# Kernel tuning notes

Hardware: AMD Instinct MI355X
Metric: run time of the kernel (lower is better)

Reference implementation:

```python
import jax, jax.numpy as jnp
import numpy as np

NUM_EXPERTS = 8
TOP_K = 2
HIDDEN = 1024
INTER = 4096
LB_WEIGHT = 0.01


def setup_inputs() -> dict:
    key = jax.random.key(0)
    ks = jax.random.split(key, 6)
    s = 0.02
    return {
        "hidden_states": jax.random.normal(ks[0], (2, 2048, HIDDEN), dtype=jnp.float32),
        "Wg": jax.random.normal(ks[1], (HIDDEN, NUM_EXPERTS), dtype=jnp.float32) * s,
        "w1": jax.random.normal(ks[2], (NUM_EXPERTS, HIDDEN, INTER), dtype=jnp.float32) * s,
        "b1": jnp.zeros((NUM_EXPERTS, INTER), dtype=jnp.float32),
        "w2": jax.random.normal(ks[3], (NUM_EXPERTS, INTER, HIDDEN), dtype=jnp.float32) * s,
        "b2": jnp.zeros((NUM_EXPERTS, HIDDEN), dtype=jnp.float32),
    }


def reference(hidden_states, Wg, w1, b1, w2, b2):
    B, S, H = hidden_states.shape
    x = hidden_states.reshape(-1, H)            # [T, H]
    T = x.shape[0]

    # 1. Gating: softmax over experts, top-k selection, renormalized gates
    probs = jax.nn.softmax(x @ Wg, axis=-1)     # [T, E]
    top_v, top_i = jax.lax.top_k(probs, TOP_K)  # [T, K]
    gate = top_v / jnp.sum(top_v, axis=-1, keepdims=True)

    # Load-balancing aux loss: E * sum(frac_assigned * mean_prob) * weight
    frac = jnp.mean(jax.nn.one_hot(top_i, NUM_EXPERTS, dtype=probs.dtype), axis=(0, 1))  # [E]
    mean_p = jnp.mean(probs, axis=0)            # [E]
    aux_loss = NUM_EXPERTS * jnp.sum(frac * mean_p) * LB_WEIGHT

    # Combine weights: per-token weight for each expert (sum of matching top-k gates)
    combine = jnp.zeros((T, NUM_EXPERTS), dtype=x.dtype)
    combine = combine.at[jnp.arange(T)[:, None], top_i].add(gate)  # [T, E]

    # 2-4. Expert FFN + weighted combine (math-equivalent dense-per-expert form)
    out = jnp.zeros_like(x)
    for e in range(NUM_EXPERTS):
        h = jax.nn.gelu(x @ w1[e] + b1[e])       # [T, INTER]
        out = out + combine[:, e:e + 1] * (h @ w2[e] + b2[e])
    return out.reshape(B, S, H), aux_loss
```

## Files before the change

### kernel.cpp

```cpp
#include <hip/hip_runtime.h>
#include <hip/hip_bf16.h>

#define T_TOK   4096
#define HID     1024
#define INTER   4096
#define NEXP    8
#define MAXT    72
#define MAXSLOT 9216
#define TPB_TOK 16

typedef __attribute__((ext_vector_type(8))) short s16x8;
typedef __attribute__((ext_vector_type(4))) float f32x4;

__device__ __forceinline__ void load_lds16(const void* g, void* l) {
    __builtin_amdgcn_global_load_lds(
        (const __attribute__((address_space(1))) void*)g,
        (__attribute__((address_space(3))) void*)l, 16, 0, 0);
}

__device__ __forceinline__ float gelu_tanh(float v) {
    float c = 0.7978845608028654f;
    float u = v + 0.044715f * v * v * v;
    return 0.5f * v * (1.0f + tanhf(c * u));
}

__global__ void transpose_bf16_kernel(const float* __restrict__ in, __hip_bfloat16* __restrict__ out,
                                      int R, int C) {
    __shared__ float tile[32][33];
    size_t eoff = (size_t)blockIdx.z * R * C;
    int c0 = blockIdx.x * 32, r0 = blockIdx.y * 32;
    int tx = threadIdx.x & 31, ty = threadIdx.x >> 5;
    #pragma unroll
    for (int i = 0; i < 32; i += 8)
        tile[ty + i][tx] = in[eoff + (size_t)(r0 + ty + i) * C + c0 + tx];
    __syncthreads();
    #pragma unroll
    for (int i = 0; i < 32; i += 8)
        out[eoff + (size_t)(c0 + ty + i) * R + r0 + tx] = __float2bfloat16(tile[tx][ty + i]);
}

__global__ void gating_kernel(const float* __restrict__ x, const float* __restrict__ Wg,
                              __hip_bfloat16* __restrict__ xb,
                              float* __restrict__ combine, int* __restrict__ counts,
                              float* __restrict__ prob_sums, int* __restrict__ idxcap) {
    __shared__ float s_ps[NEXP];
    __shared__ int   s_cnt[NEXP];
    __shared__ int   s_base[NEXP];
    __shared__ int   s_ei[TPB_TOK][2];
    __shared__ int   s_rk[TPB_TOK][2];

    int tid = threadIdx.x, wv = tid >> 6, ln = tid & 63;
    if (tid < NEXP) { s_ps[tid] = 0.f; s_cnt[tid] = 0; }
    __syncthreads();

    int t0 = blockIdx.x * TPB_TOK;
    for (int sub = 0; sub < 4; ++sub) {
        int tl = wv * 4 + sub;
        int t = t0 + tl;
        const float* xr = x + (size_t)t * HID + ln * 16;
        float4 xv[4];
        #pragma unroll
        for (int i = 0; i < 4; ++i) xv[i] = *(const float4*)(xr + i * 4);

        __hip_bfloat16 row[16];
        #pragma unroll
        for (int i = 0; i < 4; ++i) {
            row[i * 4 + 0] = __float2bfloat16(xv[i].x);
            row[i * 4 + 1] = __float2bfloat16(xv[i].y);
            row[i * 4 + 2] = __float2bfloat16(xv[i].z);
            row[i * 4 + 3] = __float2bfloat16(xv[i].w);
        }
        __hip_bfloat16* xbr = xb + (size_t)t * HID + ln * 16;
        *(s16x8*)(xbr)     = *(s16x8*)&row[0];
        *(s16x8*)(xbr + 8) = *(s16x8*)&row[8];

        float acc[NEXP] = {0,0,0,0,0,0,0,0};
        #pragma unroll
        for (int i = 0; i < 4; ++i) {
            float xs[4] = {xv[i].x, xv[i].y, xv[i].z, xv[i].w};
            #pragma unroll
            for (int j = 0; j < 4; ++j) {
                int k = ln * 16 + i * 4 + j;
                float4 wa = *(const float4*)(Wg + (size_t)k * 8);
                float4 wb = *(const float4*)(Wg + (size_t)k * 8 + 4);
                acc[0] += xs[j] * wa.x; acc[1] += xs[j] * wa.y;
                acc[2] += xs[j] * wa.z; acc[3] += xs[j] * wa.w;
                acc[4] += xs[j] * wb.x; acc[5] += xs[j] * wb.y;
                acc[6] += xs[j] * wb.z; acc[7] += xs[j] * wb.w;
            }
        }
        #pragma unroll
        for (int e = 0; e < NEXP; ++e)
            #pragma unroll
            for (int off = 32; off >= 1; off >>= 1)
                acc[e] += __shfl_xor(acc[e], off);

        float m = acc[0];
        #pragma unroll
        for (int e = 1; e < NEXP; ++e) m = fmaxf(m, acc[e]);
        float p[NEXP], s = 0.f;
        #pragma unroll
        for (int e = 0; e < NEXP; ++e) { p[e] = __expf(acc[e] - m); s += p[e]; }
        float inv = 1.0f / s;
        #pragma unroll
        for (int e = 0; e < NEXP; ++e) p[e] *= inv;

        int i0 = 0;
        #pragma unroll
        for (int e = 1; e < NEXP; ++e) if (p[e] > p[i0]) i0 = e;
        int i1 = (i0 == 0) ? 1 : 0;
        #pragma unroll
        for (int e = 0; e < NEXP; ++e) if (e != i0 && p[e] > p[i1]) i1 = e;
        float gs = p[i0] + p[i1];
        float g0 = p[i0] / gs, g1 = p[i1] / gs;

        if (ln == 0) {
            float rowc[NEXP] = {0,0,0,0,0,0,0,0};
            rowc[i0] = g0; rowc[i1] = g1;
            float4* cr = (float4*)(combine + (size_t)t * NEXP);
            cr[0] = make_float4(rowc[0], rowc[1], rowc[2], rowc[3]);
            cr[1] = make_float4(rowc[4], rowc[5], rowc[6], rowc[7]);
            #pragma unroll
            for (int e = 0; e < NEXP; ++e) atomicAdd(&s_ps[e], p[e]);
            int r0 = atomicAdd(&s_cnt[i0], 1);
            int r1 = atomicAdd(&s_cnt[i1], 1);
            s_ei[tl][0] = i0; s_rk[tl][0] = r0;
            s_ei[tl][1] = i1; s_rk[tl][1] = r1;
        }
    }
    __syncthreads();
    if (tid < NEXP) {
        s_base[tid] = atomicAdd(&counts[tid], s_cnt[tid]);
        atomicAdd(&prob_sums[tid], s_ps[tid]);
    }
    __syncthreads();
    if (tid < TPB_TOK * 2) {
        int tl = tid >> 1, k = tid & 1;
        int e = s_ei[tl][k];
        idxcap[e * T_TOK + s_base[e] + s_rk[tl][k]] = t0 + tl;
    }
}

__global__ void plan_kernel(const int* __restrict__ counts, const float* __restrict__ prob_sums,
                            int* __restrict__ offs, int* __restrict__ tile_e,
                            int* __restrict__ tile_s0, int* __restrict__ tile_nv,
                            int* __restrict__ ntiles, float* __restrict__ aux_out) {
    int tt = 0, o = 0;
    for (int e = 0; e < NEXP; ++e) {
        offs[e] = o;
        int n = counts[e];
        int nt = (n + 127) >> 7;
        for (int r = 0; r < nt; ++r) {
            tile_e[tt] = e;
            tile_s0[tt] = o + r * 128;
            int nv = n - r * 128; if (nv > 128) nv = 128;
            tile_nv[tt] = nv;
            ++tt;
        }
        o += nt * 128;
    }
    *ntiles = tt;
    float aux = 0.f;
    for (int e = 0; e < NEXP; ++e)
        aux += ((float)counts[e] / (float)(T_TOK * 2)) * (prob_sums[e] / (float)T_TOK);
    aux_out[0] = (float)NEXP * aux * 0.01f;
}

__global__ void compact_kernel(const int* __restrict__ counts, const int* __restrict__ offs,
                               const int* __restrict__ tile_e, const int* __restrict__ tile_s0,
                               const int* __restrict__ ntiles,
                               const int* __restrict__ idxcap, int* __restrict__ idxc) {
    int tt = blockIdx.x;
    if (tt >= *ntiles) return;
    int e = tile_e[tt];
    int slot = tile_s0[tt] + threadIdx.x;
    int i = slot - offs[e];
    int n = counts[e];
    idxc[slot] = (i < n) ? idxcap[e * T_TOK + i] : 0;
}

__global__ __launch_bounds__(256, 2)
void gemm1_kernel(const __hip_bfloat16* __restrict__ xb,
                  const __hip_bfloat16* __restrict__ w1b,
                  const float* __restrict__ b1,
                  const int* __restrict__ idxc,
                  const int* __restrict__ tile_e, const int* __restrict__ tile_s0,
                  const int* __restrict__ ntiles,
                  __hip_bfloat16* __restrict__ h)
{
    int tt = blockIdx.x;
    if (tt >= *ntiles) return;
    int e = tile_e[tt];
    int slot0 = tile_s0[tt];
    int n0 = blockIdx.y * 128;

    __shared__ __hip_bfloat16 As[128][32];
    __shared__ __hip_bfloat16 Bs[128][32];
    __shared__ int s_idx[128];

    int tid = threadIdx.x, wv = tid >> 6, ln = tid & 63;
    if (tid < 128) s_idx[tid] = idxc[slot0 + tid];
    __syncthreads();

    int rA0 = (wv * 2 + 0) * 16 + (ln >> 2);
    int rA1 = rA0 + 16;
    const __hip_bfloat16* srcA0 = xb + (size_t)s_idx[rA0] * HID + (ln & 3) * 8;
    const __hip_bfloat16* srcA1 = xb + (size_t)s_idx[rA1] * HID + (ln & 3) * 8;
    const __hip_bfloat16* wbase = w1b + (size_t)e * INTER * HID;
    const __hip_bfloat16* srcB0 = wbase + (size_t)(n0 + rA0) * HID + (ln & 3) * 8;
    const __hip_bfloat16* srcB1 = wbase + (size_t)(n0 + rA1) * HID + (ln & 3) * 8;
    char* ldsA0 = (char*)&As[0][0] + (wv * 2 + 0) * 1024;
    char* ldsA1 = (char*)&As[0][0] + (wv * 2 + 1) * 1024;
    char* ldsB0 = (char*)&Bs[0][0] + (wv * 2 + 0) * 1024;
    char* ldsB1 = (char*)&Bs[0][0] + (wv * 2 + 1) * 1024;

    f32x4 acc[4][4] = {};
    int wr = wv >> 1, wc = wv & 1;
    int lr = ln & 15, kb = (ln >> 4) * 8;

    for (int kt = 0; kt < HID; kt += 32) {
        load_lds16(srcA0 + kt, ldsA0);
        load_lds16(srcA1 + kt, ldsA1);
        load_lds16(srcB0 + kt, ldsB0);
        load_lds16(srcB1 + kt, ldsB1);
        __syncthreads();
        s16x8 af[4], bf[4];
        #pragma unroll
        for (int m = 0; m < 4; ++m) af[m] = *(const s16x8*)&As[wr * 64 + m * 16 + lr][kb];
        #pragma unroll
        for (int n = 0; n < 4; ++n) bf[n] = *(const s16x8*)&Bs[wc * 64 + n * 16 + lr][kb];
        #pragma unroll
        for (int m = 0; m < 4; ++m)
            #pragma unroll
            for (int n = 0; n < 4; ++n)
                acc[m][n] = __builtin_amdgcn_mfma_f32_16x16x32_bf16(af[m], bf[n], acc[m][n], 0, 0, 0);
        __syncthreads();
    }

    const float* b1e = b1 + (size_t)e * INTER;
    int rq = (ln >> 4) * 4;
    #pragma unroll
    for (int m = 0; m < 4; ++m) {
        #pragma unroll
        for (int r = 0; r < 4; ++r) {
            int row = wr * 64 + m * 16 + rq + r;
            size_t hrow = (size_t)(slot0 + row) * INTER;
            #pragma unroll
            for (int n = 0; n < 4; ++n) {
                int col = n0 + wc * 64 + n * 16 + lr;
                float v = acc[m][n][r] + b1e[col];
                h[hrow + col] = __float2bfloat16(gelu_tanh(v));
            }
        }
    }
}

__global__ __launch_bounds__(256, 2)
void gemm2_kernel(const __hip_bfloat16* __restrict__ h,
                  const __hip_bfloat16* __restrict__ w2b,
                  const float* __restrict__ b2,
                  const float* __restrict__ combine,
                  const int* __restrict__ idxc,
                  const int* __restrict__ tile_e, const int* __restrict__ tile_s0,
                  const int* __restrict__ tile_nv, const int* __restrict__ ntiles,
                  float* __restrict__ out)
{
    int tt = blockIdx.x;
    if (tt >= *ntiles) return;
    int e = tile_e[tt];
    int slot0 = tile_s0[tt];
    int n0 = blockIdx.y * 128;

    __shared__ __hip_bfloat16 As[128][32];
    __shared__ __hip_bfloat16 Bs[128][32];
    __shared__ int s_idx[128];

    int tid = threadIdx.x, wv = tid >> 6, ln = tid & 63;
    if (tid < 128) s_idx[tid] = idxc[slot0 + tid];
    __syncthreads();

    int rA0 = (wv * 2 + 0) * 16 + (ln >> 2);
    int rA1 = rA0 + 16;
    const __hip_bfloat16* srcA0 = h + (size_t)(slot0 + rA0) * INTER + (ln & 3) * 8;
    const __hip_bfloat16* srcA1 = h + (size_t)(slot0 + rA1) * INTER + (ln & 3) * 8;
    const __hip_bfloat16* wbase = w2b + (size_t)e * HID * INTER;
    const __hip_bfloat16* srcB0 = wbase + (size_t)(n0 + rA0) * INTER + (ln & 3) * 8;
    const __hip_bfloat16* srcB1 = wbase + (size_t)(n0 + rA1) * INTER + (ln & 3) * 8;
    char* ldsA0 = (char*)&As[0][0] + (wv * 2 + 0) * 1024;
    char* ldsA1 = (char*)&As[0][0] + (wv * 2 + 1) * 1024;
    char* ldsB0 = (char*)&Bs[0][0] + (wv * 2 + 0) * 1024;
    char* ldsB1 = (char*)&Bs[0][0] + (wv * 2 + 1) * 1024;

    f32x4 acc[4][4] = {};
    int wr = wv >> 1, wc = wv & 1;
    int lr = ln & 15, kb = (ln >> 4) * 8;

    for (int kt = 0; kt < INTER; kt += 32) {
        load_lds16(srcA0 + kt, ldsA0);
        load_lds16(srcA1 + kt, ldsA1);
        load_lds16(srcB0 + kt, ldsB0);
        load_lds16(srcB1 + kt, ldsB1);
        __syncthreads();
        s16x8 af[4], bf[4];
        #pragma unroll
        for (int m = 0; m < 4; ++m) af[m] = *(const s16x8*)&As[wr * 64 + m * 16 + lr][kb];
        #pragma unroll
        for (int n = 0; n < 4; ++n) bf[n] = *(const s16x8*)&Bs[wc * 64 + n * 16 + lr][kb];
        #pragma unroll
        for (int m = 0; m < 4; ++m)
            #pragma unroll
            for (int n = 0; n < 4; ++n)
                acc[m][n] = __builtin_amdgcn_mfma_f32_16x16x32_bf16(af[m], bf[n], acc[m][n], 0, 0, 0);
        __syncthreads();
    }

    const float* b2e = b2 + (size_t)e * HID;
    int nv = tile_nv[tt];
    int rq = (ln >> 4) * 4;
    #pragma unroll
    for (int m = 0; m < 4; ++m) {
        #pragma unroll
        for (int r = 0; r < 4; ++r) {
            int row = wr * 64 + m * 16 + rq + r;
            if (row < nv) {
                int tok = s_idx[row];
                float g = combine[(size_t)tok * 8 + e];
                #pragma unroll
                for (int n = 0; n < 4; ++n) {
                    int col = n0 + wc * 64 + n * 16 + lr;
                    float v = acc[m][n][r] + b2e[col];
                    atomicAdd(&out[(size_t)tok * HID + col], g * v);
                }
            }
        }
    }
}

static const size_t OFF_XB      = 0;
static const size_t SZ_XB       = (size_t)T_TOK * HID * 2;
static const size_t OFF_W1B     = OFF_XB + SZ_XB;
static const size_t SZ_W        = (size_t)NEXP * INTER * HID * 2;
static const size_t OFF_W2B     = OFF_W1B + SZ_W;
static const size_t OFF_H       = OFF_W2B + SZ_W;
static const size_t SZ_H        = (size_t)MAXSLOT * INTER * 2;
static const size_t OFF_COMBINE = OFF_H + SZ_H;
static const size_t OFF_IDXCAP  = OFF_COMBINE + (size_t)T_TOK * 8 * 4;
static const size_t OFF_IDXC    = OFF_IDXCAP + (size_t)NEXP * T_TOK * 4;
static const size_t OFF_COUNTS  = OFF_IDXC + (size_t)MAXSLOT * 4;
static const size_t OFF_PSUMS   = OFF_COUNTS + 32;
static const size_t OFF_OFFS    = OFF_PSUMS + 32;
static const size_t OFF_TILE_E  = OFF_OFFS + 64;
static const size_t OFF_TILE_S0 = OFF_TILE_E + 512;
static const size_t OFF_TILE_NV = OFF_TILE_S0 + 512;
static const size_t OFF_NTILES  = OFF_TILE_NV + 512;

extern "C" void kernel_launch(void* const* d_in, const int* in_sizes, int n_in,
                              void* d_out, int out_size, void* d_ws, size_t ws_size,
                              hipStream_t stream) {
    const float* x  = (const float*)d_in[0];
    const float* Wg = (const float*)d_in[1];
    const float* w1 = (const float*)d_in[2];
    const float* b1 = (const float*)d_in[3];
    const float* w2 = (const float*)d_in[4];
    const float* b2 = (const float*)d_in[5];
    float* out = (float*)d_out;
    char* ws = (char*)d_ws;

    __hip_bfloat16* xb   = (__hip_bfloat16*)(ws + OFF_XB);
    __hip_bfloat16* w1b  = (__hip_bfloat16*)(ws + OFF_W1B);
    __hip_bfloat16* w2b  = (__hip_bfloat16*)(ws + OFF_W2B);
    __hip_bfloat16* h    = (__hip_bfloat16*)(ws + OFF_H);
    float* combine       = (float*)(ws + OFF_COMBINE);
    int*   idxcap        = (int*)(ws + OFF_IDXCAP);
    int*   idxc          = (int*)(ws + OFF_IDXC);
    int*   counts        = (int*)(ws + OFF_COUNTS);
    float* psums         = (float*)(ws + OFF_PSUMS);
    int*   offs          = (int*)(ws + OFF_OFFS);
    int*   tile_e        = (int*)(ws + OFF_TILE_E);
    int*   tile_s0       = (int*)(ws + OFF_TILE_S0);
    int*   tile_nv       = (int*)(ws + OFF_TILE_NV);
    int*   ntiles        = (int*)(ws + OFF_NTILES);

    (void)hipMemsetAsync(out, 0, (size_t)out_size * sizeof(float), stream);
    (void)hipMemsetAsync(ws + OFF_COUNTS, 0, 64, stream);

    transpose_bf16_kernel<<<dim3(INTER / 32, HID / 32, NEXP), 256, 0, stream>>>(w1, w1b, HID, INTER);
    transpose_bf16_kernel<<<dim3(HID / 32, INTER / 32, NEXP), 256, 0, stream>>>(w2, w2b, INTER, HID);
    gating_kernel<<<T_TOK / TPB_TOK, 256, 0, stream>>>(x, Wg, xb, combine, counts, psums, idxcap);
    plan_kernel<<<1, 1, 0, stream>>>(counts, psums, offs, tile_e, tile_s0, tile_nv, ntiles,
                                     out + (size_t)T_TOK * HID);
    compact_kernel<<<MAXT, 128, 0, stream>>>(counts, offs, tile_e, tile_s0, ntiles, idxcap, idxc);
    gemm1_kernel<<<dim3(MAXT, INTER / 128), 256, 0, stream>>>(xb, w1b, b1, idxc, tile_e, tile_s0,
                                                              ntiles, h);
    gemm2_kernel<<<dim3(MAXT, HID / 128), 256, 0, stream>>>(h, w2b, b2, combine, idxc, tile_e,
                                                            tile_s0, tile_nv, ntiles, out);
}
```

Baseline: 433.7 us.

## Double-buffer LDS with BK=64, XOR swizzle, and XCD-aware block remapping in expert GEMMs

Both expert GEMM kernels now use a K-tile of 64 with two LDS buffers, so the global-to-LDS loads for the next tile are issued before computing on the current one, and the loop needs one barrier per iteration instead of two. The LDS layout gets an XOR swizzle on the 16-byte chunks to reduce bank conflicts on the MFMA fragment reads. The 2D grid is flattened and remapped so that consecutive blocks on each XCD work on the same expert tile, aiming for better L2 reuse of the weights. LDS use grows from 16KB to 64KB per block, which may cut occupancy below the two blocks per CU that the launch bounds request.

```diff
diff --git a/kernel.cpp b/kernel.cpp
--- a/kernel.cpp
+++ b/kernel.cpp
@@ -179,6 +179,7 @@
     idxc[slot] = (i < n) ? idxcap[e * T_TOK + i] : 0;
 }
 
+
 __global__ __launch_bounds__(256, 2)
 void gemm1_kernel(const __hip_bfloat16* __restrict__ xb,
                   const __hip_bfloat16* __restrict__ w1b,
@@ -188,53 +189,76 @@
                   const int* __restrict__ ntiles,
                   __hip_bfloat16* __restrict__ h)
 {
-    int tt = blockIdx.x;
+    const int NWG = MAXT * (INTER / 128);
+    int bid = blockIdx.x;
+    int w = (bid & 7) * (NWG / 8) + (bid >> 3);
+    int tt = w >> 5;
+    int n0 = (w & 31) * 128;
     if (tt >= *ntiles) return;
     int e = tile_e[tt];
     int slot0 = tile_s0[tt];
-    int n0 = blockIdx.y * 128;
-
-    __shared__ __hip_bfloat16 As[128][32];
-    __shared__ __hip_bfloat16 Bs[128][32];
+
+    __shared__ __hip_bfloat16 As[2][128][64];
+    __shared__ __hip_bfloat16 Bs[2][128][64];
     __shared__ int s_idx[128];
 
     int tid = threadIdx.x, wv = tid >> 6, ln = tid & 63;
     if (tid < 128) s_idx[tid] = idxc[slot0 + tid];
     __syncthreads();
 
-    int rA0 = (wv * 2 + 0) * 16 + (ln >> 2);
-    int rA1 = rA0 + 16;
-    const __hip_bfloat16* srcA0 = xb + (size_t)s_idx[rA0] * HID + (ln & 3) * 8;
-    const __hip_bfloat16* srcA1 = xb + (size_t)s_idx[rA1] * HID + (ln & 3) * 8;
+    int swz = ((ln & 7) ^ (ln >> 3)) * 8;
+    const __hip_bfloat16* srcA[4];
+    const __hip_bfloat16* srcB[4];
     const __hip_bfloat16* wbase = w1b + (size_t)e * INTER * HID;
-    const __hip_bfloat16* srcB0 = wbase + (size_t)(n0 + rA0) * HID + (ln & 3) * 8;
-    const __hip_bfloat16* srcB1 = wbase + (size_t)(n0 + rA1) * HID + (ln & 3) * 8;
-    char* ldsA0 = (char*)&As[0][0] + (wv * 2 + 0) * 1024;
-    char* ldsA1 = (char*)&As[0][0] + (wv * 2 + 1) * 1024;
-    char* ldsB0 = (char*)&Bs[0][0] + (wv * 2 + 0) * 1024;
-    char* ldsB1 = (char*)&Bs[0][0] + (wv * 2 + 1) * 1024;
+    #pragma unroll
+    for (int j = 0; j < 4; ++j) {
+        int r = wv * 32 + j * 8 + (ln >> 3);
+        srcA[j] = xb + (size_t)s_idx[r] * HID + swz;
+        srcB[j] = wbase + (size_t)(n0 + r) * HID + swz;
+    }
 
     f32x4 acc[4][4] = {};
-    int wr = wv >> 1, wc = wv & 1;
-    int lr = ln & 15, kb = (ln >> 4) * 8;
-
-    for (int kt = 0; kt < HID; kt += 32) {
-        load_lds16(srcA0 + kt, ldsA0);
-        load_lds16(srcA1 + kt, ldsA1);
-        load_lds16(srcB0 + kt, ldsB0);
-        load_lds16(srcB1 + kt, ldsB1);
+    int wr = wv >> 1, wc = wv & 1, lr = ln & 15;
+
+    auto STAGE = [&](int b, int kt) {
+        #pragma unroll
+        for (int j = 0; j < 4; ++j) {
+            load_lds16(srcA[j] + kt, (void*)&As[b][wv * 32 + j * 8][0]);
+            load_lds16(srcB[j] + kt, (void*)&Bs[b][wv * 32 + j * 8][0]);
+        }
+    };
+    auto COMPUTE = [&](int b) {
+        #pragma unroll
+        for (int kk = 0; kk < 2; ++kk) {
+            int lslot = (((kk * 4) + (ln >> 4)) ^ (ln & 7)) * 16;
+            s16x8 af[4], bf[4];
+            #pragma unroll
+            for (int m = 0; m < 4; ++m) {
+                int row = wr * 64 + m * 16 + lr;
+                af[m] = *(const s16x8*)((const char*)&As[b][0][0] + row * 128 + lslot);
+            }
+            #pragma unroll
+            for (int n = 0; n < 4; ++n) {
+                int row = wc * 64 + n * 16 + lr;
+                bf[n] = *(const s16x8*)((const char*)&Bs[b][0][0] + row * 128 + lslot);
+            }
+            #pragma unroll
+            for (int m = 0; m < 4; ++m)
+                #pragma unroll
+                for (int n = 0; n < 4; ++n)
+                    acc[m][n] = __builtin_amdgcn_mfma_f32_16x16x32_bf16(af[m], bf[n], acc[m][n], 0, 0, 0);
+        }
+    };
+
+    STAGE(0, 0);
+    __syncthreads();
+    int cur = 0;
+    const int NT = HID / 64;
+    for (int t = 0; t < NT; ++t) {
+        if (t + 1 < NT) STAGE(cur ^ 1, (t + 1) * 64);
+        COMPUTE(cur);
         __syncthreads();
-        s16x8 af[4], bf[4];
-        #pragma unroll
-        for (int m = 0; m < 4; ++m) af[m] = *(const s16x8*)&As[wr * 64 + m * 16 + lr][kb];
-        #pragma unroll
-        for (int n = 0; n < 4; ++n) bf[n] = *(const s16x8*)&Bs[wc * 64 + n * 16 + lr][kb];
-        #pragma unroll
-        for (int m = 0; m < 4; ++m)
-            #pragma unroll
-            for (int n = 0; n < 4; ++n)
-                acc[m][n] = __builtin_amdgcn_mfma_f32_16x16x32_bf16(af[m], bf[n], acc[m][n], 0, 0, 0);
-        __syncthreads();
+        cur ^= 1;
     }
 
     const float* b1e = b1 + (size_t)e * INTER;
@@ -265,53 +289,75 @@
                   const int* __restrict__ tile_nv, const int* __restrict__ ntiles,
                   float* __restrict__ out)
 {
-    int tt = blockIdx.x;
+    const int NWG = MAXT * (HID / 128);
+    int bid = blockIdx.x;
+    int w = (bid & 7) * (NWG / 8) + (bid >> 3);
+    int tt = w >> 3;
+    int n0 = (w & 7) * 128;
     if (tt >= *ntiles) return;
     int e = tile_e[tt];
     int slot0 = tile_s0[tt];
-    int n0 = blockIdx.y * 128;
-
-    __shared__ __hip_bfloat16 As[128][32];
-    __shared__ __hip_bfloat16 Bs[128][32];
+
+    __shared__ __hip_bfloat16 As[2][128][64];
+    __shared__ __hip_bfloat16 Bs[2][128][64];
     __shared__ int s_idx[128];
 
     int tid = threadIdx.x, wv = tid >> 6, ln = tid & 63;
     if (tid < 128) s_idx[tid] = idxc[slot0 + tid];
-    __syncthreads();
-
-    int rA0 = (wv * 2 + 0) * 16 + (ln >> 2);
-    int rA1 = rA0 + 16;
-    const __hip_bfloat16* srcA0 = h + (size_t)(slot0 + rA0) * INTER + (ln & 3) * 8;
-    const __hip_bfloat16* srcA1 = h + (size_t)(slot0 + rA1) * INTER + (ln & 3) * 8;
+
+    int swz = ((ln & 7) ^ (ln >> 3)) * 8;
+    const __hip_bfloat16* srcA[4];
+    const __hip_bfloat16* srcB[4];
     const __hip_bfloat16* wbase = w2b + (size_t)e * HID * INTER;
-    const __hip_bfloat16* srcB0 = wbase + (size_t)(n0 + rA0) * INTER + (ln & 3) * 8;
-    const __hip_bfloat16* srcB1 = wbase + (size_t)(n0 + rA1) * INTER + (ln & 3) * 8;
-    char* ldsA0 = (char*)&As[0][0] + (wv * 2 + 0) * 1024;
-    char* ldsA1 = (char*)&As[0][0] + (wv * 2 + 1) * 1024;
-    char* ldsB0 = (char*)&Bs[0][0] + (wv * 2 + 0) * 1024;
-    char* ldsB1 = (char*)&Bs[0][0] + (wv * 2 + 1) * 1024;
+    #pragma unroll
+    for (int j = 0; j < 4; ++j) {
+        int r = wv * 32 + j * 8 + (ln >> 3);
+        srcA[j] = h + (size_t)(slot0 + r) * INTER + swz;
+        srcB[j] = wbase + (size_t)(n0 + r) * INTER + swz;
+    }
 
     f32x4 acc[4][4] = {};
-    int wr = wv >> 1, wc = wv & 1;
-    int lr = ln & 15, kb = (ln >> 4) * 8;
-
-    for (int kt = 0; kt < INTER; kt += 32) {
-        load_lds16(srcA0 + kt, ldsA0);
-        load_lds16(srcA1 + kt, ldsA1);
-        load_lds16(srcB0 + kt, ldsB0);
-        load_lds16(srcB1 + kt, ldsB1);
+    int wr = wv >> 1, wc = wv & 1, lr = ln & 15;
+
+    auto STAGE = [&](int b, int kt) {
+        #pragma unroll
+        for (int j = 0; j < 4; ++j) {
+            load_lds16(srcA[j] + kt, (void*)&As[b][wv * 32 + j * 8][0]);
+            load_lds16(srcB[j] + kt, (void*)&Bs[b][wv * 32 + j * 8][0]);
+        }
+    };
+    auto COMPUTE = [&](int b) {
+        #pragma unroll
+        for (int kk = 0; kk < 2; ++kk) {
+            int lslot = (((kk * 4) + (ln >> 4)) ^ (ln & 7)) * 16;
+            s16x8 af[4], bf[4];
+            #pragma unroll
+            for (int m = 0; m < 4; ++m) {
+                int row = wr * 64 + m * 16 + lr;
+                af[m] = *(const s16x8*)((const char*)&As[b][0][0] + row * 128 + lslot);
+            }
+            #pragma unroll
+            for (int n = 0; n < 4; ++n) {
+                int row = wc * 64 + n * 16 + lr;
+                bf[n] = *(const s16x8*)((const char*)&Bs[b][0][0] + row * 128 + lslot);
+            }
+            #pragma unroll
+            for (int m = 0; m < 4; ++m)
+                #pragma unroll
+                for (int n = 0; n < 4; ++n)
+                    acc[m][n] = __builtin_amdgcn_mfma_f32_16x16x32_bf16(af[m], bf[n], acc[m][n], 0, 0, 0);
+        }
+    };
+
+    STAGE(0, 0);
+    __syncthreads();
+    int cur = 0;
+    const int NT = INTER / 64;
+    for (int t = 0; t < NT; ++t) {
+        if (t + 1 < NT) STAGE(cur ^ 1, (t + 1) * 64);
+        COMPUTE(cur);
         __syncthreads();
-        s16x8 af[4], bf[4];
-        #pragma unroll
-        for (int m = 0; m < 4; ++m) af[m] = *(const s16x8*)&As[wr * 64 + m * 16 + lr][kb];
-        #pragma unroll
-        for (int n = 0; n < 4; ++n) bf[n] = *(const s16x8*)&Bs[wc * 64 + n * 16 + lr][kb];
-        #pragma unroll
-        for (int m = 0; m < 4; ++m)
-            #pragma unroll
-            for (int n = 0; n < 4; ++n)
-                acc[m][n] = __builtin_amdgcn_mfma_f32_16x16x32_bf16(af[m], bf[n], acc[m][n], 0, 0, 0);
-        __syncthreads();
+        cur ^= 1;
     }
 
     const float* b2e = b2 + (size_t)e * HID;
@@ -390,8 +436,8 @@
     plan_kernel<<<1, 1, 0, stream>>>(counts, psums, offs, tile_e, tile_s0, tile_nv, ntiles,
                                      out + (size_t)T_TOK * HID);
     compact_kernel<<<MAXT, 128, 0, stream>>>(counts, offs, tile_e, tile_s0, ntiles, idxcap, idxc);
-    gemm1_kernel<<<dim3(MAXT, INTER / 128), 256, 0, stream>>>(xb, w1b, b1, idxc, tile_e, tile_s0,
-                                                              ntiles, h);
-    gemm2_kernel<<<dim3(MAXT, HID / 128), 256, 0, stream>>>(h, w2b, b2, combine, idxc, tile_e,
-                                                            tile_s0, tile_nv, ntiles, out);
-}
+    gemm1_kernel<<<MAXT * (INTER / 128), 256, 0, stream>>>(xb, w1b, b1, idxc, tile_e, tile_s0,
+                                                           ntiles, h);
+    gemm2_kernel<<<MAXT * (HID / 128), 256, 0, stream>>>(h, w2b, b2, combine, idxc, tile_e,
+                                                         tile_s0, tile_nv, ntiles, out);
+}
```

New measurement: 462.3 us. 1.07x slower.
